# Optimization experiments

Measured on AMD Instinct MI355X. Metric: run time of the kernel, lower is better.

## Reference

```python
import jax, jax.numpy as jnp
import numpy as np

N_USERS = 50000
N_PRODS = 50000
N_NODES = N_USERS + N_PRODS
N_EDGES = 600000
UD, PD, H, O = 64, 100, 128, 16


def _gcn_conv(x, W, b, src, dst, n):
    """PyG GCNConv: linear transform, add self-loops, sym-normalized scatter-add."""
    x = x @ W                                    # [n, H]
    loop = jnp.arange(n, dtype=src.dtype)
    src = jnp.concatenate([src, loop])
    dst = jnp.concatenate([dst, loop])
    deg = jax.ops.segment_sum(jnp.ones_like(dst, dtype=x.dtype), dst, num_segments=n)
    dinv = jnp.where(deg > 0, jax.lax.rsqrt(deg), 0.0)
    norm = dinv[src] * dinv[dst]                 # [E+n]
    msg = x[src] * norm[:, None]                 # gather + scale
    out = jax.ops.segment_sum(msg, dst, num_segments=n)
    return out + b


def setup_inputs() -> dict:
    key = jax.random.key(0)
    ks = jax.random.split(key, 16)
    s = 0.05
    return {
        "user_feats": jax.random.normal(ks[0], (N_USERS, UD), dtype=jnp.float32),
        "prod_feats": jax.random.normal(ks[1], (N_PRODS, PD), dtype=jnp.float32),
        "edge_index": jax.random.randint(ks[2], (2, N_EDGES), 0, N_NODES, dtype=jnp.int64),
        "Wu": jax.random.normal(ks[3], (UD, H), dtype=jnp.float32) * s,
        "bu": jnp.zeros((H,), dtype=jnp.float32),
        "Wp": jax.random.normal(ks[4], (PD, H), dtype=jnp.float32) * s,
        "bp": jnp.zeros((H,), dtype=jnp.float32),
        "W1": jax.random.normal(ks[5], (H, H), dtype=jnp.float32) * s,
        "b1": jnp.zeros((H,), dtype=jnp.float32),
        "W2": jax.random.normal(ks[6], (H, H), dtype=jnp.float32) * s,
        "b2": jnp.zeros((H,), dtype=jnp.float32),
        "W3": jax.random.normal(ks[7], (H, H), dtype=jnp.float32) * s,
        "b3": jnp.zeros((H,), dtype=jnp.float32),
        "Wo": jax.random.normal(ks[8], (H, O), dtype=jnp.float32) * s,
        "bo": jnp.zeros((O,), dtype=jnp.float32),
    }


def reference(user_feats, prod_feats, edge_index, Wu, bu, Wp, bp,
              W1, b1, W2, b2, W3, b3, Wo, bo):
    src, dst = edge_index[0], edge_index[1]
    user_x = user_feats @ Wu + bu
    prod_x = prod_feats @ Wp + bp
    x = jnp.concatenate([user_x, prod_x], axis=0)   # [N_NODES, H]
    x = jax.nn.relu(_gcn_conv(x, W1, b1, src, dst, N_NODES))
    # dropout p=0.6 is identity in eval mode
    x = jax.nn.relu(_gcn_conv(x, W2, b2, src, dst, N_NODES))
    x = jax.nn.relu(_gcn_conv(x, W3, b3, src, dst, N_NODES))
    return x @ Wo + bo                              # [N_NODES, O]
```

## Files before the change

kernel.cpp:

```cpp
#include <hip/hip_runtime.h>
#include <hip/hip_fp16.h>

#define NU 50000
#define NP 50000
#define NN 100000
#define NE 600000
#define H  128
#define O  16

typedef __attribute__((ext_vector_type(8))) _Float16 half8;
typedef __attribute__((ext_vector_type(4))) _Float16 h4v;
typedef __attribute__((ext_vector_type(4))) float f32x4;

__global__ void k_prep(const float* __restrict__ Wu, const float* __restrict__ Wp,
                       const float* __restrict__ W1, const float* __restrict__ W2,
                       const float* __restrict__ W3, const float* __restrict__ Wo,
                       const float* __restrict__ user, const float* __restrict__ prod,
                       const float* __restrict__ bu, const float* __restrict__ bp,
                       __half* __restrict__ whU1, __half* __restrict__ wlU1,
                       __half* __restrict__ whP1, __half* __restrict__ wlP1,
                       __half* __restrict__ wh2, __half* __restrict__ wl2,
                       __half* __restrict__ wh3, __half* __restrict__ wl3,
                       __half* __restrict__ whO, __half* __restrict__ wlO,
                       float* __restrict__ bu1, float* __restrict__ bp1,
                       __half* __restrict__ xU, __half* __restrict__ xP,
                       int* __restrict__ cnt, int2* __restrict__ epack) {
    int idx = blockIdx.x * blockDim.x + threadIdx.x;
    if (idx >= 159656) {
        int i = idx - 159656;
        if (i < NU * 16) {
            int e = i * 4;
            float4 v = *(const float4*)(user + e);
            __half2 a = __floats2half2_rn(v.x, v.y);
            __half2 b = __floats2half2_rn(v.z, v.w);
            uint2 o; o.x = *(unsigned*)&a; o.y = *(unsigned*)&b;
            *(uint2*)(xU + e) = o;
        } else {
            int q = i - NU * 16;
            if (q >= NP * 32) return;
            int row = q >> 5, kq = (q & 31) * 4;
            float4 v;
            if (kq < 100) v = *(const float4*)(prod + row * 100 + kq);
            else { v.x = 0.f; v.y = 0.f; v.z = 0.f; v.w = 0.f; }
            __half2 a = __floats2half2_rn(v.x, v.y);
            __half2 b = __floats2half2_rn(v.z, v.w);
            uint2 o; o.x = *(unsigned*)&a; o.y = *(unsigned*)&b;
            *(uint2*)(xP + (size_t)row * 128 + kq) = o;
        }
        return;
    }
    if (idx >= 59648) {
        int i = idx - 59648;
        if (i < NN) cnt[i] = 0;
        else if (i < NN + 8) { int2 z; z.x = 0; z.y = 0; epack[NE + (i - NN)] = z; }
        return;
    }
    if (idx >= 59392) {
        int n = idx - 59392;
        const float* bsrc = (n < 128) ? bu : bp;
        int nn = n & 127;
        float acc = 0.f;
        for (int j = 0; j < 128; ++j) acc = fmaf(bsrc[j], W1[j * 128 + nn], acc);
        if (n < 128) bu1[nn] = acc; else bp1[nn] = acc;
        return;
    }
    float x;
    __half *Wh, *Wl; int sidx;
    if (idx < 8192) {
        int n = idx >> 6, k = idx & 63;
        float acc = 0.f;
        for (int j = 0; j < 128; ++j) acc = fmaf(Wu[k * 128 + j], W1[j * 128 + n], acc);
        x = acc * 16.0f; Wh = whU1; Wl = wlU1; sidx = idx;
    } else if (idx < 24576) {
        int l = idx - 8192;
        int n = l >> 7, k = l & 127;
        float acc = 0.f;
        if (k < 100)
            for (int j = 0; j < 128; ++j) acc = fmaf(Wp[k * 128 + j], W1[j * 128 + n], acc);
        x = acc * 16.0f; Wh = whP1; Wl = wlP1; sidx = l;
    } else if (idx < 40960) {
        int l = idx - 24576;
        int n = l >> 7, k = l & 127;
        x = W2[k * 128 + n] * 16.0f; Wh = wh2; Wl = wl2; sidx = l;
    } else if (idx < 57344) {
        int l = idx - 40960;
        int n = l >> 7, k = l & 127;
        x = W3[k * 128 + n] * 16.0f; Wh = wh3; Wl = wl3; sidx = l;
    } else {
        int l = idx - 57344;
        int n = l >> 7, k = l & 127;
        x = Wo[k * 16 + n] * 16.0f; Wh = whO; Wl = wlO; sidx = l;
    }
    __half h = __float2half_rn(x);
    __half l2 = __float2half_rn(x - __half2float(h));
    Wh[sidx] = h; Wl[sidx] = l2;
}

__global__ void k_count(const int* __restrict__ dst, int* __restrict__ cnt,
                        int* __restrict__ rank, int E) {
    int e = blockIdx.x * blockDim.x + threadIdx.x;
    if (e < E) rank[e] = atomicAdd(&cnt[dst[e]], 1);
}

#define SCAN_TPB 256
#define SCAN_VPT 4
#define SCAN_CHUNK (SCAN_TPB * SCAN_VPT)

__global__ void k_scan1(const int* __restrict__ in, int* __restrict__ out,
                        int* __restrict__ bsums, float* __restrict__ dinv, int n) {
    __shared__ int sh[SCAN_TPB];
    int t = threadIdx.x, b = blockIdx.x;
    int base = b * SCAN_CHUNK + t * SCAN_VPT;
    int v[SCAN_VPT]; int s = 0;
#pragma unroll
    for (int i = 0; i < SCAN_VPT; i++) {
        int idx = base + i;
        v[i] = (idx < n) ? in[idx] : 0;
        if (idx < n) dinv[idx] = rsqrtf((float)(v[i] + 1));
        s += v[i];
    }
    sh[t] = s; __syncthreads();
    for (int off = 1; off < SCAN_TPB; off <<= 1) {
        int x = (t >= off) ? sh[t - off] : 0;
        __syncthreads();
        sh[t] += x;
        __syncthreads();
    }
    int run = (t > 0) ? sh[t - 1] : 0;
    if (t == SCAN_TPB - 1) bsums[b] = sh[t];
#pragma unroll
    for (int i = 0; i < SCAN_VPT; i++) {
        int idx = base + i;
        if (idx < n) out[idx] = run;
        run += v[i];
    }
}

__global__ void k_scan2(int* __restrict__ bsums, int nb) {
    __shared__ int sh[128];
    int t = threadIdx.x;
    int v = (t < nb) ? bsums[t] : 0;
    sh[t] = v; __syncthreads();
    for (int off = 1; off < 128; off <<= 1) {
        int x = (t >= off) ? sh[t - off] : 0;
        __syncthreads();
        sh[t] += x;
        __syncthreads();
    }
    if (t < nb) bsums[t] = sh[t] - v;
}

template <typename AT, int K, int KPAD, int NI, int MI, int NOUT, bool BIAS, bool F32OUT>
__device__ __forceinline__
void gemm_body(const AT* __restrict__ X,
               const __half* __restrict__ Wh, const __half* __restrict__ Wl,
               const float* __restrict__ bias, void* __restrict__ Cout,
               int M, int orow0, int vb) {
    constexpr int KS = KPAD / 32;
    constexpr int CSPLIT = NOUT / (16 * MI);
    const int tid  = threadIdx.x;
    const int wid  = tid >> 6, lane = tid & 63;
    const int lm   = lane & 15, q = lane >> 4;
    const int gw   = vb * 4 + wid;
    const int tile = gw / CSPLIT;
    const int c0   = (gw % CSPLIT) * (MI * 16);
    const int NT   = (M + NI * 16 - 1) / (NI * 16);
    if (tile >= NT) return;
    const int n0 = tile * (NI * 16);

    half8 wh[MI][KS], wl[MI][KS];
#pragma unroll
    for (int mi = 0; mi < MI; mi++)
#pragma unroll
        for (int ks = 0; ks < KS; ks++) {
            const size_t b = (size_t)(c0 + mi * 16 + lm) * KPAD + ks * 32 + q * 8;
            wh[mi][ks] = *(const half8*)&Wh[b];
            wl[mi][ks] = *(const half8*)&Wl[b];
        }

    f32x4 acc[NI][MI];
#pragma unroll
    for (int ni = 0; ni < NI; ni++)
#pragma unroll
        for (int mi = 0; mi < MI; mi++) acc[ni][mi] = (f32x4)0.0f;

#pragma unroll
    for (int ni = 0; ni < NI; ni++) {
        const int node = n0 + ni * 16 + lm;
        half8 xf[KS];
        if (node < M) {
#pragma unroll
            for (int ks = 0; ks < KS; ks++)
                xf[ks] = *(const half8*)((const __half*)X + (size_t)node * KPAD + ks * 32 + q * 8);
        } else {
#pragma unroll
            for (int ks = 0; ks < KS; ks++)
#pragma unroll
                for (int j = 0; j < 8; j++) xf[ks][j] = (_Float16)0.0f;
        }
#pragma unroll
        for (int ks = 0; ks < KS; ks++)
#pragma unroll
            for (int mi = 0; mi < MI; mi++) {
                acc[ni][mi] = __builtin_amdgcn_mfma_f32_16x16x32_f16(wh[mi][ks], xf[ks], acc[ni][mi], 0, 0, 0);
                acc[ni][mi] = __builtin_amdgcn_mfma_f32_16x16x32_f16(wl[mi][ks], xf[ks], acc[ni][mi], 0, 0, 0);
            }
    }

#pragma unroll
    for (int ni = 0; ni < NI; ni++) {
        const int node = n0 + ni * 16 + lm;
        if (node >= M) continue;
#pragma unroll
        for (int mi = 0; mi < MI; mi++) {
            const int cb = c0 + mi * 16 + q * 4;
            float4 bv = BIAS ? *(const float4*)&bias[cb] : make_float4(0.f, 0.f, 0.f, 0.f);
            float v0 = fmaf(acc[ni][mi][0], 0.0625f, bv.x);
            float v1 = fmaf(acc[ni][mi][1], 0.0625f, bv.y);
            float v2 = fmaf(acc[ni][mi][2], 0.0625f, bv.z);
            float v3 = fmaf(acc[ni][mi][3], 0.0625f, bv.w);
            if constexpr (F32OUT) {
                *(float4*)((float*)Cout + (size_t)(orow0 + node) * NOUT + cb) =
                    make_float4(v0, v1, v2, v3);
            } else {
                __half2 h0 = __floats2half2_rn(v0, v1);
                __half2 h1 = __floats2half2_rn(v2, v3);
                uint2 o; o.x = *(unsigned*)&h0; o.y = *(unsigned*)&h1;
                *(uint2*)((__half*)Cout + (size_t)(orow0 + node) * NOUT + cb) = o;
            }
        }
    }
}

template <typename AT, int K, int KPAD, int NI, int MI, int NOUT, bool BIAS, bool F32OUT>
__launch_bounds__(256)
__global__ void k_gemm_reg(const AT* __restrict__ X,
                           const __half* __restrict__ Wh, const __half* __restrict__ Wl,
                           const float* __restrict__ bias, void* __restrict__ Cout,
                           int M, int orow0) {
    gemm_body<AT, K, KPAD, NI, MI, NOUT, BIAS, F32OUT>(X, Wh, Wl, bias, Cout, M, orow0, blockIdx.x);
}

#define BLK_U 782
#define BLK_P 1563
#define BLK_F 2344
__launch_bounds__(256)
__global__ void k_fill_g1(const int* __restrict__ src, const int* __restrict__ dst,
                          const int* __restrict__ offs, const int* __restrict__ bsums,
                          const int* __restrict__ rank, const float* __restrict__ dinv,
                          int2* __restrict__ epack,
                          const __half* __restrict__ xU, const __half* __restrict__ xP,
                          const __half* __restrict__ whU1, const __half* __restrict__ wlU1,
                          const __half* __restrict__ whP1, const __half* __restrict__ wlP1,
                          const float* __restrict__ bu1, const float* __restrict__ bp1,
                          void* __restrict__ xB) {
    const int b = blockIdx.x;
    if (b < BLK_U) {
        gemm_body<__half,  64,  64, 2, 4, 128, true, false>(xU, whU1, wlU1, bu1, xB, NU, 0, b);
    } else if (b < BLK_U + BLK_P) {
        gemm_body<__half, 128, 128, 2, 2, 128, true, false>(xP, whP1, wlP1, bp1, xB, NP, NU, b - BLK_U);
    } else {
        int e = (b - BLK_U - BLK_P) * 256 + threadIdx.x;
        if (e < NE) {
            int s = src[e], d = dst[e];
            int p = offs[d] + bsums[d >> 10] + rank[e];
            int2 r;
            r.x = s;
            r.y = __float_as_int(dinv[s] * dinv[d]);
            epack[p] = r;
        }
    }
}

__launch_bounds__(256)
__global__ void k_aggregate(const __half* __restrict__ y, const int* __restrict__ offs,
                            const int* __restrict__ bsums, const int2* __restrict__ epack,
                            const float* __restrict__ dinv, const float* __restrict__ bias,
                            __half* __restrict__ out) {
    const int node = __builtin_amdgcn_readfirstlane(blockIdx.x * 4 + (threadIdx.x >> 6));
    const int l = threadIdx.x & 63;
    const int h = l >> 5, j = l & 31;

    int e0 = offs[node] + bsums[node >> 10];
    int e1 = (node + 1 < NN) ? (offs[node + 1] + bsums[(node + 1) >> 10]) : NE;
    e0 = __builtin_amdgcn_readfirstlane(e0);
    e1 = __builtin_amdgcn_readfirstlane(e1);

    const h4v* y4 = (const h4v*)y;

    const float di2 = dinv[node] * dinv[node];
    h4v sv = y4[(size_t)node * 32 + j];
    float4 bv = *(const float4*)&bias[4 * j];

    f32x4 acc0 = (f32x4)0.f, acc1 = (f32x4)0.f, acc2 = (f32x4)0.f, acc3 = (f32x4)0.f;

    for (int e = e0; e < e1; e += 8) {
        const int eb = e + 4 * h;
        const int2* pe = epack + eb;
        int2 p0 = pe[0];
        int2 p1 = pe[1];
        int2 p2 = pe[2];
        int2 p3 = pe[3];
        const bool k0 = (eb + 0 < e1), k1 = (eb + 1 < e1);
        const bool k2 = (eb + 2 < e1), k3 = (eb + 3 < e1);
        float w0 = k0 ? __int_as_float(p0.y) : 0.f;
        float w1 = k1 ? __int_as_float(p1.y) : 0.f;
        float w2 = k2 ? __int_as_float(p2.y) : 0.f;
        float w3 = k3 ? __int_as_float(p3.y) : 0.f;
        const int s0 = k0 ? p0.x : node;
        const int s1 = k1 ? p1.x : node;
        const int s2 = k2 ? p2.x : node;
        const int s3 = k3 ? p3.x : node;
        h4v v0 = y4[(size_t)s0 * 32 + j];
        h4v v1 = y4[(size_t)s1 * 32 + j];
        h4v v2 = y4[(size_t)s2 * 32 + j];
        h4v v3 = y4[(size_t)s3 * 32 + j];
        acc0[0] = fmaf((float)v0[0], w0, acc0[0]); acc0[1] = fmaf((float)v0[1], w0, acc0[1]);
        acc0[2] = fmaf((float)v0[2], w0, acc0[2]); acc0[3] = fmaf((float)v0[3], w0, acc0[3]);
        acc1[0] = fmaf((float)v1[0], w1, acc1[0]); acc1[1] = fmaf((float)v1[1], w1, acc1[1]);
        acc1[2] = fmaf((float)v1[2], w1, acc1[2]); acc1[3] = fmaf((float)v1[3], w1, acc1[3]);
        acc2[0] = fmaf((float)v2[0], w2, acc2[0]); acc2[1] = fmaf((float)v2[1], w2, acc2[1]);
        acc2[2] = fmaf((float)v2[2], w2, acc2[2]); acc2[3] = fmaf((float)v2[3], w2, acc2[3]);
        acc3[0] = fmaf((float)v3[0], w3, acc3[0]); acc3[1] = fmaf((float)v3[1], w3, acc3[1]);
        acc3[2] = fmaf((float)v3[2], w3, acc3[2]); acc3[3] = fmaf((float)v3[3], w3, acc3[3]);
    }

    f32x4 s = (acc0 + acc1) + (acc2 + acc3);
    float t0 = s[0] + __shfl_xor(s[0], 32, 64);
    float t1 = s[1] + __shfl_xor(s[1], 32, 64);
    float t2 = s[2] + __shfl_xor(s[2], 32, 64);
    float t3 = s[3] + __shfl_xor(s[3], 32, 64);

    float r0 = fmaf((float)sv[0], di2, t0) + bv.x;
    float r1 = fmaf((float)sv[1], di2, t1) + bv.y;
    float r2 = fmaf((float)sv[2], di2, t2) + bv.z;
    float r3 = fmaf((float)sv[3], di2, t3) + bv.w;
    if (l < 32) {
        __half2 ha = __floats2half2_rn(fmaxf(r0, 0.f), fmaxf(r1, 0.f));
        __half2 hb = __floats2half2_rn(fmaxf(r2, 0.f), fmaxf(r3, 0.f));
        uint2 o; o.x = *(unsigned*)&ha; o.y = *(unsigned*)&hb;
        *(uint2*)(out + (size_t)node * H + 4 * j) = o;
    }
}

extern "C" void kernel_launch(void* const* d_in, const int* in_sizes, int n_in,
                              void* d_out, int out_size, void* d_ws, size_t ws_size,
                              hipStream_t stream) {
    const float* user = (const float*)d_in[0];
    const float* prod = (const float*)d_in[1];
    const int*   eidx = (const int*)  d_in[2];
    const int*   edst = eidx + NE;
    const int*   esrc = eidx;
    const float* Wu = (const float*)d_in[3];
    const float* bu = (const float*)d_in[4];
    const float* Wp = (const float*)d_in[5];
    const float* bp = (const float*)d_in[6];
    const float* W1 = (const float*)d_in[7];
    const float* b1 = (const float*)d_in[8];
    const float* W2 = (const float*)d_in[9];
    const float* b2 = (const float*)d_in[10];
    const float* W3 = (const float*)d_in[11];
    const float* b3 = (const float*)d_in[12];
    const float* Wo = (const float*)d_in[13];
    const float* bo = (const float*)d_in[14];
    float* out = (float*)d_out;

    char* ws = (char*)d_ws;
    size_t p = 0;
    auto alloc = [&](size_t bytes) -> void* {
        void* r = ws + p;
        p += (bytes + 255) & ~(size_t)255;
        return r;
    };
    __half* xA   = (__half*)alloc((size_t)NN * H * 2);
    __half* xB   = (__half*)alloc((size_t)NN * H * 2);
    __half* xU   = (__half*)alloc((size_t)NU * 64 * 2);
    __half* xP   = (__half*)alloc((size_t)NP * 128 * 2);
    int*   cnt   = (int*)  alloc((size_t)NN * 4);
    int*   rank  = (int*)  alloc((size_t)NE * 4);
    int*   offs  = (int*)  alloc((size_t)(NN + 1) * 4);
    float* dinv  = (float*)alloc((size_t)NN * 4);
    int2*  epack = (int2*) alloc((size_t)(NE + 8) * 8);
    int*   bsums = (int*)  alloc(128 * 4);
    __half* whU1 = (__half*)alloc(128 * 64 * 2);
    __half* wlU1 = (__half*)alloc(128 * 64 * 2);
    __half* whP1 = (__half*)alloc(128 * 128 * 2);
    __half* wlP1 = (__half*)alloc(128 * 128 * 2);
    __half* wh2 = (__half*)alloc(128 * 128 * 2);
    __half* wl2 = (__half*)alloc(128 * 128 * 2);
    __half* wh3 = (__half*)alloc(128 * 128 * 2);
    __half* wl3 = (__half*)alloc(128 * 128 * 2);
    __half* whO = (__half*)alloc(16 * 128 * 2);
    __half* wlO = (__half*)alloc(16 * 128 * 2);
    float* bu1  = (float*)alloc(128 * 4);
    float* bp1  = (float*)alloc(128 * 4);

    const int NBLK = (NN + SCAN_CHUNK - 1) / SCAN_CHUNK;

    {
        const int total = 159656 + NU * 16 + NP * 32;
        k_prep<<<(total + 255) / 256, 256, 0, stream>>>(
            Wu, Wp, W1, W2, W3, Wo, user, prod, bu, bp,
            whU1, wlU1, whP1, wlP1, wh2, wl2, wh3, wl3, whO, wlO,
            bu1, bp1, xU, xP, cnt, epack);
    }

    k_count<<<(NE + 255) / 256, 256, 0, stream>>>(edst, cnt, rank, NE);
    k_scan1<<<NBLK, SCAN_TPB, 0, stream>>>(cnt, offs, bsums, dinv, NN);
    k_scan2<<<1, 128, 0, stream>>>(bsums, NBLK);

    k_fill_g1<<<BLK_U + BLK_P + BLK_F, 256, 0, stream>>>(
        esrc, edst, offs, bsums, rank, dinv, epack,
        xU, xP, whU1, wlU1, whP1, wlP1, bu1, bp1, xB);

    const int blkG = (1563 * 2 + 3) / 4;
    const int blkO = (1563 + 3) / 4;

    k_aggregate<<<NN / 4, 256, 0, stream>>>(xB, offs, bsums, epack, dinv, b1, xA);
    k_gemm_reg<__half, 128, 128, 4, 4, 128, false, false><<<blkG, 256, 0, stream>>>(xA, wh2, wl2, nullptr, xB, NN, 0);
    k_aggregate<<<NN / 4, 256, 0, stream>>>(xB, offs, bsums, epack, dinv, b2, xA);
    k_gemm_reg<__half, 128, 128, 4, 4, 128, false, false><<<blkG, 256, 0, stream>>>(xA, wh3, wl3, nullptr, xB, NN, 0);
    k_aggregate<<<NN / 4, 256, 0, stream>>>(xB, offs, bsums, epack, dinv, b3, xA);

    k_gemm_reg<__half, 128, 128, 4, 1, 16, true, true><<<blkO, 256, 0, stream>>>(xA, whO, wlO, bo, out, NN, 0);
}
```

Baseline: 264.0 us.

## Fold edge degree counting into prep kernel and enlarge layer-1 GEMM tiles

The separate k_count kernel is removed and its atomic degree counting becomes another index range of k_prep. The cnt zeroing moves to a hipMemsetAsync issued before k_prep, so counting can share a launch with the feature and weight conversion. The first-layer user and product GEMMs in k_fill_g1 now use a larger NI tile, which halves their block counts. This saves one kernel launch and improves GEMM reuse, at the cost of an extra memset call and more register pressure per GEMM block.

```diff
diff --git a/kernel.cpp b/kernel.cpp
--- a/kernel.cpp
+++ b/kernel.cpp
@@ -17,6 +17,7 @@
                        const float* __restrict__ W3, const float* __restrict__ Wo,
                        const float* __restrict__ user, const float* __restrict__ prod,
                        const float* __restrict__ bu, const float* __restrict__ bp,
+                       const int* __restrict__ edst,
                        __half* __restrict__ whU1, __half* __restrict__ wlU1,
                        __half* __restrict__ whP1, __half* __restrict__ wlP1,
                        __half* __restrict__ wh2, __half* __restrict__ wl2,
@@ -24,35 +25,38 @@
                        __half* __restrict__ whO, __half* __restrict__ wlO,
                        float* __restrict__ bu1, float* __restrict__ bp1,
                        __half* __restrict__ xU, __half* __restrict__ xP,
-                       int* __restrict__ cnt, int2* __restrict__ epack) {
+                       int* __restrict__ cnt, int* __restrict__ rank,
+                       int2* __restrict__ epack) {
     int idx = blockIdx.x * blockDim.x + threadIdx.x;
-    if (idx >= 159656) {
-        int i = idx - 159656;
-        if (i < NU * 16) {
-            int e = i * 4;
-            float4 v = *(const float4*)(user + e);
-            __half2 a = __floats2half2_rn(v.x, v.y);
-            __half2 b = __floats2half2_rn(v.z, v.w);
-            uint2 o; o.x = *(unsigned*)&a; o.y = *(unsigned*)&b;
-            *(uint2*)(xU + e) = o;
-        } else {
-            int q = i - NU * 16;
-            if (q >= NP * 32) return;
-            int row = q >> 5, kq = (q & 31) * 4;
-            float4 v;
-            if (kq < 100) v = *(const float4*)(prod + row * 100 + kq);
-            else { v.x = 0.f; v.y = 0.f; v.z = 0.f; v.w = 0.f; }
-            __half2 a = __floats2half2_rn(v.x, v.y);
-            __half2 b = __floats2half2_rn(v.z, v.w);
-            uint2 o; o.x = *(unsigned*)&a; o.y = *(unsigned*)&b;
-            *(uint2*)(xP + (size_t)row * 128 + kq) = o;
-        }
+    if (idx >= 2459656) {
+        int e = idx - 2459656;
+        if (e < NE) rank[e] = atomicAdd(&cnt[edst[e]], 1);
         return;
     }
+    if (idx >= 859656) {
+        int q = idx - 859656;
+        int row = q >> 5, kq = (q & 31) * 4;
+        float4 v;
+        if (kq < 100) v = *(const float4*)(prod + row * 100 + kq);
+        else { v.x = 0.f; v.y = 0.f; v.z = 0.f; v.w = 0.f; }
+        __half2 a = __floats2half2_rn(v.x, v.y);
+        __half2 b = __floats2half2_rn(v.z, v.w);
+        uint2 o; o.x = *(unsigned*)&a; o.y = *(unsigned*)&b;
+        *(uint2*)(xP + (size_t)row * 128 + kq) = o;
+        return;
+    }
+    if (idx >= 59656) {
+        int e = (idx - 59656) * 4;
+        float4 v = *(const float4*)(user + e);
+        __half2 a = __floats2half2_rn(v.x, v.y);
+        __half2 b = __floats2half2_rn(v.z, v.w);
+        uint2 o; o.x = *(unsigned*)&a; o.y = *(unsigned*)&b;
+        *(uint2*)(xU + e) = o;
+        return;
+    }
     if (idx >= 59648) {
-        int i = idx - 59648;
-        if (i < NN) cnt[i] = 0;
-        else if (i < NN + 8) { int2 z; z.x = 0; z.y = 0; epack[NE + (i - NN)] = z; }
+        int2 z; z.x = 0; z.y = 0;
+        epack[NE + (idx - 59648)] = z;
         return;
     }
     if (idx >= 59392) {
@@ -96,12 +100,6 @@
     Wh[sidx] = h; Wl[sidx] = l2;
 }
 
-__global__ void k_count(const int* __restrict__ dst, int* __restrict__ cnt,
-                        int* __restrict__ rank, int E) {
-    int e = blockIdx.x * blockDim.x + threadIdx.x;
-    if (e < E) rank[e] = atomicAdd(&cnt[dst[e]], 1);
-}
-
 #define SCAN_TPB 256
 #define SCAN_VPT 4
 #define SCAN_CHUNK (SCAN_TPB * SCAN_VPT)
@@ -241,8 +239,8 @@
     gemm_body<AT, K, KPAD, NI, MI, NOUT, BIAS, F32OUT>(X, Wh, Wl, bias, Cout, M, orow0, blockIdx.x);
 }
 
-#define BLK_U 782
-#define BLK_P 1563
+#define BLK_U 391
+#define BLK_P 782
 #define BLK_F 2344
 __launch_bounds__(256)
 __global__ void k_fill_g1(const int* __restrict__ src, const int* __restrict__ dst,
@@ -256,9 +254,9 @@
                           void* __restrict__ xB) {
     const int b = blockIdx.x;
     if (b < BLK_U) {
-        gemm_body<__half,  64,  64, 2, 4, 128, true, false>(xU, whU1, wlU1, bu1, xB, NU, 0, b);
+        gemm_body<__half,  64,  64, 4, 4, 128, true, false>(xU, whU1, wlU1, bu1, xB, NU, 0, b);
     } else if (b < BLK_U + BLK_P) {
-        gemm_body<__half, 128, 128, 2, 2, 128, true, false>(xP, whP1, wlP1, bp1, xB, NP, NU, b - BLK_U);
+        gemm_body<__half, 128, 128, 4, 2, 128, true, false>(xP, whP1, wlP1, bp1, xB, NP, NU, b - BLK_U);
     } else {
         int e = (b - BLK_U - BLK_P) * 256 + threadIdx.x;
         if (e < NE) {
@@ -397,15 +395,15 @@
 
     const int NBLK = (NN + SCAN_CHUNK - 1) / SCAN_CHUNK;
 
+    hipMemsetAsync(cnt, 0, (size_t)NN * 4, stream);
     {
-        const int total = 159656 + NU * 16 + NP * 32;
+        const int total = 2459656 + NE;
         k_prep<<<(total + 255) / 256, 256, 0, stream>>>(
-            Wu, Wp, W1, W2, W3, Wo, user, prod, bu, bp,
+            Wu, Wp, W1, W2, W3, Wo, user, prod, bu, bp, edst,
             whU1, wlU1, whP1, wlP1, wh2, wl2, wh3, wl3, whO, wlO,
-            bu1, bp1, xU, xP, cnt, epack);
-    }
-
-    k_count<<<(NE + 255) / 256, 256, 0, stream>>>(edst, cnt, rank, NE);
+            bu1, bp1, xU, xP, cnt, rank, epack);
+    }
+
     k_scan1<<<NBLK, SCAN_TPB, 0, stream>>>(cnt, offs, bsums, dinv, NN);
     k_scan2<<<1, 128, 0, stream>>>(bsums, NBLK);
 
```

After: 257.5 us. 1.03x faster.
